# Kernel tuning notes

Hardware: AMD Instinct MI355X
Metric: run time of the kernel (lower is better)

The kernel has to match this reference:

```python
import jax, jax.numpy as jnp
import numpy as np

ALPHA = 20.0  # SuperSpike surrogate sharpness
V_TH = 1.0
DT = 1.0

@jax.custom_vjp
def heaviside(x):
    return (x > 0).astype(x.dtype)

def _heaviside_fwd(x):
    return heaviside(x), x

def _heaviside_bwd(x, g):
    # SuperSpike surrogate gradient: 1 / (alpha*|x| + 1)^2
    return (g / (ALPHA * jnp.abs(x) + 1.0) ** 2,)

heaviside.defvjp(_heaviside_fwd, _heaviside_bwd)


def setup_inputs() -> dict:
    key = jax.random.key(0)
    k1, k2 = jax.random.split(key)
    B, T, IN, H = 128, 2000, 16, 256
    x = jax.random.normal(k1, (B, T, IN), dtype=jnp.float32)
    W = jax.random.normal(k2, (H, IN), dtype=jnp.float32) / np.sqrt(IN)
    tau_syn = jnp.full((1, H), 0.1, dtype=jnp.float32)
    tau_mem = jnp.full((1, H), 0.05, dtype=jnp.float32)
    return {"x": x, "W": W, "tau_syn": tau_syn, "tau_mem": tau_mem}


def reference(x, W, tau_syn, tau_mem):
    """SNNEncode forward: linear input projection + LIF recurrence over time.
    x: [B,T,IN], W: [H,IN], taus: [1,H]. Returns (spikes [T,B,H], (v,i) final state)."""
    tau_syn_inv = jnp.clip(tau_syn, 0.0, 1.0)  # [1,H]
    tau_mem_inv = jnp.clip(tau_mem, 0.0, 1.0)  # [1,H]

    B, T, IN = x.shape
    H = W.shape[0]
    # project all timesteps at once: [T,B,H]
    xw = jnp.einsum("bti,hi->tbh", x, W)

    def step(state, inp_t):
        v, i = state
        # norse lif_feed_forward_step (v_leak = 0, v_reset = 0)
        v_dec = v + DT * tau_mem_inv * (-v + i)
        i_dec = i + DT * (-tau_syn_inv) * i
        z = heaviside(v_dec - V_TH)
        v_new = (1.0 - z) * v_dec
        i_new = i_dec + inp_t
        return (v_new, i_new), z

    zeros = jnp.zeros((B, H), dtype=x.dtype)
    (v_f, i_f), spikes = jax.lax.scan(step, (zeros, zeros), xw)
    return spikes, v_f, i_f
```

## Files before the change

### kernel.cpp

```cpp
#include <hip/hip_runtime.h>


constexpr int B  = 128;
constexpr int T  = 2000;
constexpr int IN = 16;
constexpr int H  = 256;
constexpr int TC = 128;
constexpr int NCH = (T + TC - 1) / TC;
constexpr int BH = B * H;

__global__ __launch_bounds__(128, 1) void snn_np_blas(
    const float* __restrict__ x, const float* __restrict__ Wm,
    const float* __restrict__ tau_syn, const float* __restrict__ tau_mem,
    float* __restrict__ out)
{
#pragma clang fp contract(off)
  __shared__ float xs[TC * IN];
  const int tid = threadIdx.x;
  const int bid = blockIdx.x;
  const int b = bid >> 1;
  const int h = ((bid & 1) << 7) | tid;

  float w[IN];
#pragma unroll
  for (int k = 0; k < IN; ++k) w[k] = Wm[h * IN + k];

  float ts = tau_syn[h];
  ts = ts < 0.f ? 0.f : (ts > 1.f ? 1.f : ts);
  float tm = tau_mem[h];
  tm = tm < 0.f ? 0.f : (tm > 1.f ? 1.f : tm);
  const float nts = -ts;

  const float* xb = x + (size_t)b * T * IN;
  float* op = out + (size_t)b * H + h;

  float vS = 0.f, iS = 0.f;

  for (int c = 0; c < NCH; ++c) {
    const int t0   = c * TC;
    const int rows = min(TC, T - t0);
    const int n    = rows * IN;

    __syncthreads();
    for (int idx = tid; idx < n; idx += 128)
      xs[idx] = xb[t0 * IN + idx];
    __syncthreads();

    for (int r = 0; r < rows; ++r) {
      const float* xr = xs + r * IN;

      float acc = 0.0f;
#pragma unroll
      for (int k = 0; k < IN; ++k)
        acc = __builtin_fmaf(xr[k], w[k], acc);
      const float xw = acc;

      const float t1 = iS - vS;
      const float t2 = tm * t1;
      const float vd = vS + t2;
      const float xm = vd - 1.0f;
      const bool  sp = xm > 0.0f;
      vS = sp ? 0.0f : vd;
      const float t3 = nts * iS;
      const float id = iS + t3;
      iS = id + xw;

      __builtin_nontemporal_store(sp ? 1.0f : 0.0f, op);
      op += BH;
    }
  }

  out[(size_t)T * BH + (size_t)b * H + h]      = vS;
  out[(size_t)T * BH + BH + (size_t)b * H + h] = iS;
}

extern "C" void kernel_launch(void* const* d_in, const int* in_sizes, int n_in,
                              void* d_out, int out_size, void* d_ws, size_t ws_size,
                              hipStream_t stream) {
  const float* x  = (const float*)d_in[0];
  const float* W  = (const float*)d_in[1];
  const float* ts = (const float*)d_in[2];
  const float* tm = (const float*)d_in[3];
  float* out = (float*)d_out;
  hipLaunchKernelGGL(snn_np_blas, dim3(B * 2), dim3(128), 0, stream,
                     x, W, ts, tm, out);
}
```

Measured before the change: 450.0 us.

## Replace shared-memory chunk staging with register double-buffered projection pipeline

Result: slower. 869.8 us (+93.3%).

```diff
diff --git a/kernel.cpp b/kernel.cpp
--- a/kernel.cpp
+++ b/kernel.cpp
@@ -5,17 +5,15 @@
 constexpr int T  = 2000;
 constexpr int IN = 16;
 constexpr int H  = 256;
-constexpr int TC = 128;
-constexpr int NCH = (T + TC - 1) / TC;
 constexpr int BH = B * H;
+constexpr int NB = 8;
 
-__global__ __launch_bounds__(128, 1) void snn_np_blas(
+__global__ __launch_bounds__(128, 1) void snn_pipe(
     const float* __restrict__ x, const float* __restrict__ Wm,
     const float* __restrict__ tau_syn, const float* __restrict__ tau_mem,
     float* __restrict__ out)
 {
 #pragma clang fp contract(off)
-  __shared__ float xs[TC * IN];
   const int tid = threadIdx.x;
   const int bid = blockIdx.x;
   const int b = bid >> 1;
@@ -36,25 +34,23 @@
 
   float vS = 0.f, iS = 0.f;
 
-  for (int c = 0; c < NCH; ++c) {
-    const int t0   = c * TC;
-    const int rows = min(TC, T - t0);
-    const int n    = rows * IN;
+  float xwA[NB], xwB[NB];
 
-    __syncthreads();
-    for (int idx = tid; idx < n; idx += 128)
-      xs[idx] = xb[t0 * IN + idx];
-    __syncthreads();
-
-    for (int r = 0; r < rows; ++r) {
-      const float* xr = xs + r * IN;
-
+  auto CX = [&](float* xw, int t0) {
+#pragma unroll
+    for (int j = 0; j < NB; ++j) {
+      const float* xr = xb + (size_t)(t0 + j) * IN;
       float acc = 0.0f;
 #pragma unroll
       for (int k = 0; k < IN; ++k)
         acc = __builtin_fmaf(xr[k], w[k], acc);
-      const float xw = acc;
+      xw[j] = acc;
+    }
+  };
 
+  auto LIF = [&](const float* xw) {
+#pragma unroll
+    for (int j = 0; j < NB; ++j) {
       const float t1 = iS - vS;
       const float t2 = tm * t1;
       const float vd = vS + t2;
@@ -63,11 +59,18 @@
       vS = sp ? 0.0f : vd;
       const float t3 = nts * iS;
       const float id = iS + t3;
-      iS = id + xw;
-
+      iS = id + xw[j];
       __builtin_nontemporal_store(sp ? 1.0f : 0.0f, op);
       op += BH;
     }
+  };
+
+  CX(xwA, 0);
+  for (int t0 = 0; t0 < T; t0 += 2 * NB) {
+    CX(xwB, t0 + NB);
+    LIF(xwA);
+    if (t0 + 2 * NB < T) CX(xwA, t0 + 2 * NB);
+    LIF(xwB);
   }
 
   out[(size_t)T * BH + (size_t)b * H + h]      = vS;
@@ -82,6 +85,6 @@
   const float* ts = (const float*)d_in[2];
   const float* tm = (const float*)d_in[3];
   float* out = (float*)d_out;
-  hipLaunchKernelGGL(snn_np_blas, dim3(B * 2), dim3(128), 0, stream,
+  hipLaunchKernelGGL(snn_pipe, dim3(B * 2), dim3(128), 0, stream,
                      x, W, ts, tm, out);
 }
```

## Use packed FMAs over interleaved timestep pairs and pipeline projection with LIF

Applied to the files above, without the earlier changes.

Measured after the change: 393.7 us. -12.5%, faster.

```diff
diff --git a/kernel.cpp b/kernel.cpp
--- a/kernel.cpp
+++ b/kernel.cpp
@@ -9,7 +9,14 @@
 constexpr int NCH = (T + TC - 1) / TC;
 constexpr int BH = B * H;
 
-__global__ __launch_bounds__(128, 1) void snn_np_blas(
+typedef float f2 __attribute__((ext_vector_type(2)));
+typedef float f4 __attribute__((ext_vector_type(4)));
+
+static __device__ __forceinline__ f2 fma2(f2 a, f2 b, f2 c) {
+  return __builtin_elementwise_fma(a, b, c);
+}
+
+__global__ __launch_bounds__(128, 1) void snn_pk(
     const float* __restrict__ x, const float* __restrict__ Wm,
     const float* __restrict__ tau_syn, const float* __restrict__ tau_mem,
     float* __restrict__ out)
@@ -36,25 +43,26 @@
 
   float vS = 0.f, iS = 0.f;
 
-  for (int c = 0; c < NCH; ++c) {
-    const int t0   = c * TC;
-    const int rows = min(TC, T - t0);
-    const int n    = rows * IN;
+  const f2* xsp = reinterpret_cast<const f2*>(xs);
 
-    __syncthreads();
-    for (int idx = tid; idx < n; idx += 128)
-      xs[idx] = xb[t0 * IN + idx];
-    __syncthreads();
+  auto CX = [&](f2& d0, f2& d1, f2& d2, f2& d3, int bt) {
+    const f2* q = xsp + bt * 64;
+    f2 a0 = (f2)(0.f), a1 = (f2)(0.f), a2 = (f2)(0.f), a3 = (f2)(0.f);
+#pragma unroll
+    for (int k = 0; k < IN; ++k) {
+      const f2 wk = (f2)(w[k]);
+      a0 = fma2(q[k],      wk, a0);
+      a1 = fma2(q[16 + k], wk, a1);
+      a2 = fma2(q[32 + k], wk, a2);
+      a3 = fma2(q[48 + k], wk, a3);
+    }
+    d0 = a0; d1 = a1; d2 = a2; d3 = a3;
+  };
 
-    for (int r = 0; r < rows; ++r) {
-      const float* xr = xs + r * IN;
-
-      float acc = 0.0f;
+  auto LIF = [&](f2 d0, f2 d1, f2 d2, f2 d3) {
+    float xwv[8] = {d0.x, d0.y, d1.x, d1.y, d2.x, d2.y, d3.x, d3.y};
 #pragma unroll
-      for (int k = 0; k < IN; ++k)
-        acc = __builtin_fmaf(xr[k], w[k], acc);
-      const float xw = acc;
-
+    for (int j = 0; j < 8; ++j) {
       const float t1 = iS - vS;
       const float t2 = tm * t1;
       const float vd = vS + t2;
@@ -63,10 +71,41 @@
       vS = sp ? 0.0f : vd;
       const float t3 = nts * iS;
       const float id = iS + t3;
-      iS = id + xw;
-
+      iS = id + xwv[j];
       __builtin_nontemporal_store(sp ? 1.0f : 0.0f, op);
       op += BH;
+    }
+  };
+
+  f2 A0, A1, A2, A3, B0, B1, B2, B3;
+
+  for (int c = 0; c < NCH; ++c) {
+    const int t0   = c * TC;
+    const int rows = min(TC, T - t0);
+    const int nf4  = rows * IN / 4;
+
+    __syncthreads();
+    {
+      const f4* src = reinterpret_cast<const f4*>(xb + (size_t)t0 * IN);
+      for (int i4 = tid; i4 < nf4; i4 += 128) {
+        const f4 v4 = src[i4];
+        const int r  = i4 >> 2;
+        const int k0 = (i4 & 3) << 2;
+        const int base = ((r >> 1) << 5) | (r & 1);
+#pragma unroll
+        for (int e = 0; e < 4; ++e)
+          xs[base + ((k0 + e) << 1)] = v4[e];
+      }
+    }
+    __syncthreads();
+
+    const int nbat = rows >> 3;
+    CX(A0, A1, A2, A3, 0);
+    for (int bt = 0; bt < nbat; bt += 2) {
+      CX(B0, B1, B2, B3, bt + 1);
+      LIF(A0, A1, A2, A3);
+      if (bt + 2 < nbat) CX(A0, A1, A2, A3, bt + 2);
+      LIF(B0, B1, B2, B3);
     }
   }
 
@@ -82,6 +121,6 @@
   const float* ts = (const float*)d_in[2];
   const float* tm = (const float*)d_in[3];
   float* out = (float*)d_out;
-  hipLaunchKernelGGL(snn_np_blas, dim3(B * 2), dim3(128), 0, stream,
+  hipLaunchKernelGGL(snn_pk, dim3(B * 2), dim3(128), 0, stream,
                      x, W, ts, tm, out);
 }
```
